# Kernel tuning notes

Hardware: AMD Instinct MI355X
Metric: run time of the kernel (lower is better)

The kernel has to match this reference:

```python
import jax, jax.numpy as jnp
import numpy as np

B, N, DIM = 2, 2048, 1024
H, DH = 16, 64
INNER = H * DH            # 1024
FF_INNER = 4 * DIM        # 4096
EPS = 1e-5


def _layer_norm(x, g, b):
    mu = jnp.mean(x, axis=-1, keepdims=True)
    var = jnp.mean(jnp.square(x - mu), axis=-1, keepdims=True)
    return (x - mu) * jax.lax.rsqrt(var + EPS) * g + b


def _self_attention(x, wq, wk, wv, wo, bo):
    # wq/wk/wv: [INNER, DIM] (torch Linear layout, y = x @ W^T)
    b, n, _ = x.shape
    q = jnp.einsum('bnd,id->bni', x, wq).reshape(b, n, H, DH).transpose(0, 2, 1, 3)
    k = jnp.einsum('bnd,id->bni', x, wk).reshape(b, n, H, DH).transpose(0, 2, 1, 3)
    v = jnp.einsum('bnd,id->bni', x, wv).reshape(b, n, H, DH).transpose(0, 2, 1, 3)
    scale = DH ** -0.5
    sim = jnp.einsum('bhid,bhjd->bhij', q, k) * scale   # [B,H,N,N]
    attn = jax.nn.softmax(sim, axis=-1)
    out = jnp.einsum('bhij,bhjd->bhid', attn, v)
    out = out.transpose(0, 2, 1, 3).reshape(b, n, INNER)
    return jnp.einsum('bni,di->bnd', out, wo) + bo


def _geglu_ff(x, w1, b1, w2, b2):
    # w1: [2*FF_INNER, DIM], w2: [DIM, FF_INNER]
    h = jnp.einsum('bnd,id->bni', x, w1) + b1
    a, gate = jnp.split(h, 2, axis=-1)
    h = a * jax.nn.gelu(gate, approximate=False)
    return jnp.einsum('bni,di->bnd', h, w2) + b2


def setup_inputs() -> dict:
    key = jax.random.key(0)
    ks = jax.random.split(key, 12)
    s = 0.02
    inp = {
        'x': jax.random.normal(ks[0], (B, N, DIM), jnp.float32),
        'ln1_g': jnp.ones((DIM,), jnp.float32),
        'ln1_b': jnp.zeros((DIM,), jnp.float32),
        'w_q1': jax.random.normal(ks[1], (INNER, DIM), jnp.float32) * s,
        'w_k1': jax.random.normal(ks[2], (INNER, DIM), jnp.float32) * s,
        'w_v1': jax.random.normal(ks[3], (INNER, DIM), jnp.float32) * s,
        'w_o1': jax.random.normal(ks[4], (DIM, INNER), jnp.float32) * s,
        'b_o1': jnp.zeros((DIM,), jnp.float32),
        'ln2_g': jnp.ones((DIM,), jnp.float32),
        'ln2_b': jnp.zeros((DIM,), jnp.float32),
        'w_q2': jax.random.normal(ks[5], (INNER, DIM), jnp.float32) * s,
        'w_k2': jax.random.normal(ks[6], (INNER, DIM), jnp.float32) * s,
        'w_v2': jax.random.normal(ks[7], (INNER, DIM), jnp.float32) * s,
        'w_o2': jax.random.normal(ks[8], (DIM, INNER), jnp.float32) * s,
        'b_o2': jnp.zeros((DIM,), jnp.float32),
        'ln3_g': jnp.ones((DIM,), jnp.float32),
        'ln3_b': jnp.zeros((DIM,), jnp.float32),
        'w_ff1': jax.random.normal(ks[9], (2 * FF_INNER, DIM), jnp.float32) * s,
        'b_ff1': jnp.zeros((2 * FF_INNER,), jnp.float32),
        'w_ff2': jax.random.normal(ks[10], (DIM, FF_INNER), jnp.float32) * s,
        'b_ff2': jnp.zeros((DIM,), jnp.float32),
    }
    return inp


def reference(x, ln1_g, ln1_b, w_q1, w_k1, w_v1, w_o1, b_o1,
              ln2_g, ln2_b, w_q2, w_k2, w_v2, w_o2, b_o2,
              ln3_g, ln3_b, w_ff1, b_ff1, w_ff2, b_ff2):
    # attn1 (self) + residual
    x = _self_attention(_layer_norm(x, ln1_g, ln1_b), w_q1, w_k1, w_v1, w_o1, b_o1) + x
    # attn2 (self, context=None) + residual
    x = _self_attention(_layer_norm(x, ln2_g, ln2_b), w_q2, w_k2, w_v2, w_o2, b_o2) + x
    # GEGLU feed-forward + residual
    x = _geglu_ff(_layer_norm(x, ln3_g, ln3_b), w_ff1, b_ff1, w_ff2, b_ff2) + x
    return x
```

## Files before the change

### kernel.cpp

```cpp
#include <hip/hip_runtime.h>
#include <hip/hip_bf16.h>

using bf16x8 = __attribute__((ext_vector_type(8))) short;
using f32x4  = __attribute__((ext_vector_type(4))) float;
using f32x16 = __attribute__((ext_vector_type(16))) float;
typedef unsigned int u32;
typedef unsigned short u16;
using u32x4 = __attribute__((ext_vector_type(4))) u32;

__device__ __forceinline__ u16 f2b(float f) {
  union { float f; u32 u; } v; v.f = f;
  return (u16)((v.u + 0x7FFFu + ((v.u >> 16) & 1u)) >> 16);
}

__device__ __forceinline__ u32 cvtpk(float lo, float hi) {
  u32 r;
  asm("v_cvt_pk_bf16_f32 %0, %1, %2" : "=v"(r) : "v"(lo), "v"(hi));
  return r;
}

__device__ __forceinline__ float exp2_raw(float x) {
  float r;
  asm("v_exp_f32 %0, %1" : "=v"(r) : "v"(x));
  return r;
}

__device__ __forceinline__ void gload16(const void* g, void* l) {
  __builtin_amdgcn_global_load_lds((const __attribute__((address_space(1))) u32*)g,
                                   (__attribute__((address_space(3))) u32*)l, 16, 0, 0);
}

__device__ __forceinline__ float gelu_fast(float x) {
  const float x2 = x * x;
  const float t = x * fmaf(0.044715f, x2, 1.f);
  const float u = exp2f(2.3022080f * t);
  return x * u * __builtin_amdgcn_rcpf(u + 1.f);
}

__global__ __launch_bounds__(256) void castall(
    const float* __restrict__ wq1, const float* __restrict__ wk1,
    const float* __restrict__ wv1, const float* __restrict__ wo1,
    const float* __restrict__ wq2, const float* __restrict__ wk2,
    const float* __restrict__ wv2, const float* __restrict__ wo2,
    const float* __restrict__ wff1, const float* __restrict__ wff2,
    u16* __restrict__ qkv1, u16* __restrict__ o1,
    u16* __restrict__ qkv2, u16* __restrict__ o2,
    u16* __restrict__ ff1p, u16* __restrict__ ff2) {
  const long e = ((long)blockIdx.x * 256 + threadIdx.x) * 4;
  constexpr long M1 = 1l << 20;
  const float* s; u16* d;
  if (e < 3 * M1) {
    s = (e < M1 ? wq1 + e : (e < 2 * M1 ? wk1 + (e - M1) : wv1 + (e - 2 * M1)));
    d = qkv1 + e;
  } else if (e < 4 * M1) {
    s = wo1 + (e - 3 * M1); d = o1 + (e - 3 * M1);
  } else if (e < 7 * M1) {
    long r = e - 4 * M1;
    s = (r < M1 ? wq2 + r : (r < 2 * M1 ? wk2 + (r - M1) : wv2 + (r - 2 * M1)));
    d = qkv2 + r;
  } else if (e < 8 * M1) {
    s = wo2 + (e - 7 * M1); d = o2 + (e - 7 * M1);
  } else if (e < 16 * M1) {
    long r = e - 8 * M1;
    long p = r >> 10, col = r & 1023;
    long g = p >> 5, rr = p & 31;
    long lr = (rr < 16) ? (g << 4) + rr : 4096 + (g << 4) + (rr - 16);
    s = wff1 + (lr << 10) + col; d = ff1p + r;
  } else {
    long r = e - 16 * M1;
    s = wff2 + r; d = ff2 + r;
  }
  float4 v = *(const float4*)s;
  ushort4 o;
  o.x = f2b(v.x); o.y = f2b(v.y); o.z = f2b(v.z); o.w = f2b(v.w);
  *(ushort4*)d = o;
}

__global__ __launch_bounds__(256) void ln_kernel(const float* __restrict__ x,
                                                 const float* __restrict__ g,
                                                 const float* __restrict__ b,
                                                 u16* __restrict__ y) {
  const int row = blockIdx.x;
  const int t = threadIdx.x;
  const float* xr = x + (size_t)row * 1024;
  float4 v = ((const float4*)xr)[t];
  float s  = v.x + v.y + v.z + v.w;
  float s2 = v.x * v.x + v.y * v.y + v.z * v.z + v.w * v.w;
  #pragma unroll
  for (int m = 1; m < 64; m <<= 1) {
    s  += __shfl_xor(s, m);
    s2 += __shfl_xor(s2, m);
  }
  __shared__ float red[8];
  if ((t & 63) == 0) { red[(t >> 6) * 2] = s; red[(t >> 6) * 2 + 1] = s2; }
  __syncthreads();
  s  = red[0] + red[2] + red[4] + red[6];
  s2 = red[1] + red[3] + red[5] + red[7];
  const float mu = s * (1.f / 1024.f);
  const float var = s2 * (1.f / 1024.f) - mu * mu;
  const float rs = rsqrtf(var + 1e-5f);
  float4 gv = ((const float4*)g)[t];
  float4 bv = ((const float4*)b)[t];
  ushort4 o;
  o.x = f2b((v.x - mu) * rs * gv.x + bv.x);
  o.y = f2b((v.y - mu) * rs * gv.y + bv.y);
  o.z = f2b((v.z - mu) * rs * gv.z + bv.z);
  o.w = f2b((v.w - mu) * rs * gv.w + bv.w);
  ((ushort4*)(y + (size_t)row * 1024))[t] = o;
}

__global__ __launch_bounds__(512, 4) void gemm_out(
    const u16* __restrict__ A, const u16* __restrict__ Bw,
    const float* __restrict__ bias, const float* __restrict__ resid,
    float* __restrict__ out, int N, int K) {
  extern __shared__ u16 lds[];
  const int tid = threadIdx.x;
  const int l = tid & 63, wid = tid >> 6;
  const int li = l & 15, lg = l >> 4;
  const int wr = wid >> 2, wc = wid & 3;
  const int nx = N >> 7;
  const int cpx = gridDim.x >> 3;
  const int v = (blockIdx.x & 7) * cpx + (blockIdx.x >> 3);
  const int by = v / nx, bx = v - by * nx;
  const int m0 = by << 7, n0 = bx << 7;

  const int sr = tid >> 3;
  const int sc = ((tid & 7) ^ (sr & 7)) << 3;
  const int dc = (tid & 7) << 3;
  const int sc0 = (lg * 8) ^ ((li & 7) << 3);
  const int sc1 = sc0 ^ 32;

  f32x4 acc[4][2] = {};

  auto stageA = [&](int kb, int t2) {
    #pragma unroll
    for (int s = 0; s < 2; ++s)
      gload16(A + (size_t)(m0 + s * 64 + sr) * K + t2 * 64 + sc,
              lds + kb * 8192 + (s * 64 + sr) * 64 + dc);
  };
  auto stageB = [&](int kb, int t2) {
    #pragma unroll
    for (int s = 0; s < 2; ++s)
      gload16(Bw + (size_t)(n0 + s * 64 + sr) * K + t2 * 64 + sc,
              lds + 16384 + kb * 8192 + (s * 64 + sr) * 64 + dc);
  };

  const int NT = K >> 6;
  stageA(0, 0); stageB(0, 0);
  __builtin_amdgcn_sched_barrier(0);
  stageA(1, 1); stageB(1, 1);
  __builtin_amdgcn_sched_barrier(0);
  asm volatile("s_waitcnt vmcnt(4)" ::: "memory");
  __builtin_amdgcn_s_barrier();
  __builtin_amdgcn_sched_barrier(0);

  for (int t = 0; t < NT; ++t) {
    const int kb = t & 1;
    const u16* Ab = lds + kb * 8192 + (wr * 64 + li) * 64;
    const u16* Bb = lds + 16384 + kb * 8192 + (wc * 32 + li) * 64;
    bf16x8 a[4], b[2];

    #pragma unroll
    for (int mi = 0; mi < 4; ++mi) a[mi] = *(const bf16x8*)(Ab + mi * 1024 + sc0);
    #pragma unroll
    for (int n = 0; n < 2; ++n)  b[n]  = *(const bf16x8*)(Bb + n * 1024 + sc0);
    __builtin_amdgcn_s_barrier();
    __builtin_amdgcn_s_setprio(1);
    #pragma unroll
    for (int mi = 0; mi < 4; ++mi)
      #pragma unroll
      for (int n = 0; n < 2; ++n)
        acc[mi][n] = __builtin_amdgcn_mfma_f32_16x16x32_bf16(a[mi], b[n], acc[mi][n], 0, 0, 0);
    __builtin_amdgcn_s_setprio(0);
    __builtin_amdgcn_s_barrier();

    #pragma unroll
    for (int mi = 0; mi < 4; ++mi) a[mi] = *(const bf16x8*)(Ab + mi * 1024 + sc1);
    #pragma unroll
    for (int n = 0; n < 2; ++n)  b[n]  = *(const bf16x8*)(Bb + n * 1024 + sc1);
    __builtin_amdgcn_s_barrier();
    __builtin_amdgcn_s_setprio(1);
    #pragma unroll
    for (int mi = 0; mi < 4; ++mi)
      #pragma unroll
      for (int n = 0; n < 2; ++n)
        acc[mi][n] = __builtin_amdgcn_mfma_f32_16x16x32_bf16(a[mi], b[n], acc[mi][n], 0, 0, 0);
    __builtin_amdgcn_s_setprio(0);
    if (t + 2 < NT) {
      stageA(kb, t + 2); stageB(kb, t + 2);
      asm volatile("s_waitcnt vmcnt(4)" ::: "memory");
    } else if (t + 2 == NT) {
      asm volatile("s_waitcnt vmcnt(0)" ::: "memory");
    }
    __builtin_amdgcn_s_barrier();
    __builtin_amdgcn_sched_barrier(0);
  }

  #pragma unroll
  for (int mi = 0; mi < 4; ++mi) {
    const int m = m0 + wr * 64 + mi * 16 + lg * 4;
    #pragma unroll
    for (int n = 0; n < 2; ++n) {
      const int j = n0 + wc * 32 + n * 16 + li;
      const float bj = bias[j];
      #pragma unroll
      for (int rb = 0; rb < 4; ++rb)
        out[(size_t)(m + rb) * N + j] =
            acc[mi][n][rb] + bj + resid[(size_t)(m + rb) * N + j];
    }
  }
}

#define KLOOP_PROLOGUE()                                                      \
  stageA(0, 0); stageB(0, 0); stageA(1, 0); stageB(1, 0);                     \
  __builtin_amdgcn_sched_barrier(0);                                          \
  stageA(0, 1); stageB(0, 1);                                                 \
  __builtin_amdgcn_sched_barrier(0);                                          \
  asm volatile("s_waitcnt vmcnt(4)" ::: "memory");                            \
  __builtin_amdgcn_s_barrier();                                               \
  __builtin_amdgcn_sched_barrier(0);

#define KLOOP_BODY(NT)                                                        \
  bf16x8 b0[4], b1[4];                                                        \
  for (int t = 0; t < NT; ++t) {                                              \
    const int kb = t & 1;                                                     \
    const u16* Abase0 = lds + (kb * 2 + 0) * 8192 + rowA0;                    \
    const u16* Abase1 = lds + (kb * 2 + 1) * 8192 + rowA0;                    \
    const u16* Bbase  = lds + (kb * 2 + bhn) * 8192 + rowB0;                  \
    bf16x8 a[4];                                                              \
                                                      \
    _Pragma("unroll")                                                         \
    for (int j = 0; j < 4; ++j) a[j]  = *(const bf16x8*)(Abase0 + j * 1024 + sc0); \
    _Pragma("unroll")                                                         \
    for (int n = 0; n < 4; ++n) b0[n] = *(const bf16x8*)(Bbase + n * 1024 + sc0); \
    if (t + 1 < NT) stageA(1, t + 1);                                         \
    __builtin_amdgcn_s_setprio(1);                                            \
    _Pragma("unroll")                                                         \
    for (int j = 0; j < 4; ++j)                                               \
      _Pragma("unroll")                                                       \
      for (int n = 0; n < 4; ++n)                                             \
        acc[j][n] = __builtin_amdgcn_mfma_f32_16x16x32_bf16(a[j], b0[n], acc[j][n], 0, 0, 0); \
    __builtin_amdgcn_s_setprio(0);                                            \
    __builtin_amdgcn_s_barrier();                                             \
                                                      \
    _Pragma("unroll")                                                         \
    for (int j = 0; j < 4; ++j) a[j]  = *(const bf16x8*)(Abase0 + j * 1024 + sc1); \
    _Pragma("unroll")                                                         \
    for (int n = 0; n < 4; ++n) b1[n] = *(const bf16x8*)(Bbase + n * 1024 + sc1); \
    if (t + 1 < NT) stageB(1, t + 1);                                         \
    __builtin_amdgcn_s_setprio(1);                                            \
    _Pragma("unroll")                                                         \
    for (int j = 0; j < 4; ++j)                                               \
      _Pragma("unroll")                                                       \
      for (int n = 0; n < 4; ++n)                                             \
        acc[j][n] = __builtin_amdgcn_mfma_f32_16x16x32_bf16(a[j], b1[n], acc[j][n], 0, 0, 0); \
    __builtin_amdgcn_s_setprio(0);                                            \
    __builtin_amdgcn_s_barrier();                                             \
                                                      \
    _Pragma("unroll")                                                         \
    for (int j = 0; j < 4; ++j) a[j] = *(const bf16x8*)(Abase1 + j * 1024 + sc0); \
    if (t + 2 < NT) stageA(0, t + 2);                                         \
    __builtin_amdgcn_s_setprio(1);                                            \
    _Pragma("unroll")                                                         \
    for (int j = 0; j < 4; ++j)                                               \
      _Pragma("unroll")                                                       \
      for (int n = 0; n < 4; ++n)                                             \
        acc[4 + j][n] = __builtin_amdgcn_mfma_f32_16x16x32_bf16(a[j], b0[n], acc[4 + j][n], 0, 0, 0); \
    __builtin_amdgcn_s_setprio(0);                                            \
    __builtin_amdgcn_s_barrier();                                             \
                                                      \
    _Pragma("unroll")                                                         \
    for (int j = 0; j < 4; ++j) a[j] = *(const bf16x8*)(Abase1 + j * 1024 + sc1); \
    if (t + 2 < NT) stageB(0, t + 2);                                         \
    __builtin_amdgcn_s_setprio(1);                                            \
    _Pragma("unroll")                                                         \
    for (int j = 0; j < 4; ++j)                                               \
      _Pragma("unroll")                                                       \
      for (int n = 0; n < 4; ++n)                                             \
        acc[4 + j][n] = __builtin_amdgcn_mfma_f32_16x16x32_bf16(a[j], b1[n], acc[4 + j][n], 0, 0, 0); \
    __builtin_amdgcn_s_setprio(0);                                            \
    if (t < NT - 2)       asm volatile("s_waitcnt vmcnt(4)" ::: "memory");    \
    else if (t == NT - 2) asm volatile("s_waitcnt vmcnt(0)" ::: "memory");    \
    __builtin_amdgcn_s_barrier();                                             \
  }

__global__ __launch_bounds__(512, 2) void gemm_ff1(
    const u16* __restrict__ A, const u16* __restrict__ Wp,
    const float* __restrict__ bias, u16* __restrict__ out) {
  extern __shared__ u16 lds[];
  const int tid = threadIdx.x;
  const int l = tid & 63, wid = tid >> 6;
  const int li = l & 15, lg = l >> 4;
  const int wr = wid >> 2, wc = wid & 3;
  const int xcd = blockIdx.x & 7, r = blockIdx.x >> 3;
  const int bx = (xcd & 3) * 8 + (r >> 3);
  const int by = (xcd >> 2) * 8 + (r & 7);

  const int lr8 = l >> 3;
  const int scb = ((l & 7) ^ lr8) << 3;
  const int sc0 = (lg * 8) ^ ((li & 7) << 3);
  const int sc1 = sc0 ^ 32;

  const int rowA0 = (wr * 64 + li) * 64;
  const int rowB0 = 32768 + ((wc & 1) * 64 + li) * 64;
  const int bhn = wc >> 1;

  f32x4 acc[8][4] = {};

  auto stageA = [&](int h, int t2) {
    const int kb2 = t2 & 1;
    #pragma unroll
    for (int s = 0; s < 2; ++s) {
      const u16* g = A + (size_t)(by * 256 + s * 128 + h * 64 + wid * 8 + lr8) * 1024
                       + t2 * 64 + scb;
      u16* d = lds + (kb2 * 2 + h) * 8192 + s * 4096 + wid * 512;
      gload16(g, d);
    }
  };
  auto stageB = [&](int h, int t2) {
    const int kb2 = t2 & 1;
    #pragma unroll
    for (int s = 0; s < 2; ++s) {
      const u16* g = Wp + (size_t)(bx * 256 + h * 128 + s * 64 + wid * 8 + lr8) * 1024
                        + t2 * 64 + scb;
      u16* d = lds + 32768 + (kb2 * 2 + h) * 8192 + s * 4096 + wid * 512;
      gload16(g, d);
    }
  };

  KLOOP_PROLOGUE()
  KLOOP_BODY(16)

  #pragma unroll
  for (int nj = 0; nj < 2; ++nj) {
    const int c = bx * 128 + wc * 32 + nj * 16 + li;
    const float ba = bias[c];
    const float bg = bias[4096 + c];
    #pragma unroll
    for (int mi = 0; mi < 8; ++mi) {
      #pragma unroll
      for (int rb = 0; rb < 4; ++rb) {
        const float av = acc[mi][2 * nj][rb] + ba;
        const float gv = acc[mi][2 * nj + 1][rb] + bg;
        out[(size_t)(by * 256 + wr * 128 + mi * 16 + lg * 4 + rb) * 4096 + c]
            = f2b(av * gelu_fast(gv));
      }
    }
  }
}

__global__ __launch_bounds__(512, 2) void gemm_qkv(
    const u16* __restrict__ A, const u16* __restrict__ Wp,
    u16* __restrict__ outp) {
  extern __shared__ u16 lds[];
  const int tid = threadIdx.x;
  const int l = tid & 63, wid = tid >> 6;
  const int li = l & 15, lg = l >> 4;
  const int wr = wid >> 2, wc = wid & 3;
  const int xcd = blockIdx.x & 7, r = blockIdx.x >> 3;
  const int by = (xcd >> 1) * 4 + r / 6;
  const int bx = (xcd & 1) * 6 + r % 6;

  const int lr8 = l >> 3;
  const int scb = ((l & 7) ^ lr8) << 3;
  const int sc0 = (lg * 8) ^ ((li & 7) << 3);
  const int sc1 = sc0 ^ 32;

  const int rowA0 = (wr * 64 + li) * 64;
  const int rowB0 = 32768 + ((wc & 1) * 64 + li) * 64;
  const int bhn = wc >> 1;

  f32x4 acc[8][4] = {};

  auto stageA = [&](int h, int t2) {
    const int kb2 = t2 & 1;
    #pragma unroll
    for (int s = 0; s < 2; ++s) {
      const u16* g = A + (size_t)(by * 256 + s * 128 + h * 64 + wid * 8 + lr8) * 1024
                       + t2 * 64 + scb;
      u16* d = lds + (kb2 * 2 + h) * 8192 + s * 4096 + wid * 512;
      gload16(g, d);
    }
  };
  auto stageB = [&](int h, int t2) {
    const int kb2 = t2 & 1;
    #pragma unroll
    for (int s = 0; s < 2; ++s) {
      const u16* g = Wp + (size_t)(bx * 256 + h * 128 + s * 64 + wid * 8 + lr8) * 1024
                        + t2 * 64 + scb;
      u16* d = lds + 32768 + (kb2 * 2 + h) * 8192 + s * 4096 + wid * 512;
      gload16(g, d);
    }
  };

  KLOOP_PROLOGUE()
  KLOOP_BODY(16)

  #pragma unroll
  for (int mi = 0; mi < 8; ++mi) {
    const int mbase = by * 256 + wr * 128 + mi * 16 + lg * 4;
    #pragma unroll
    for (int ni = 0; ni < 4; ++ni) {
      const int j = bx * 256 + wc * 64 + ni * 16 + li;
      f32x4 a = acc[mi][ni];
      const int sec = j >> 10, jj = j & 1023;
      const int h = jj >> 6, dd = jj & 63;
      u16* base = outp + (size_t)sec * 4194304;
      if (sec == 0) {
        #pragma unroll
        for (int rb = 0; rb < 4; ++rb) {
          const int m = mbase + rb;
          const int bb = m >> 11, n = m & 2047;
          base[(((size_t)bb * 16 + h) * 2048 + n) * 64 + dd] =
              f2b(a[rb] * 0.18033688011112042f);
        }
      } else if (sec == 1) {
        #pragma unroll
        for (int rb = 0; rb < 4; ++rb) {
          const int m = mbase + rb;
          const int bb = m >> 11, n = m & 2047;
          base[(((size_t)bb * 16 + h) * 2048 + n) * 64 + (dd ^ ((n & 7) << 3))] =
              f2b(a[rb]);
        }
      } else {
        const int bb = mbase >> 11, n = mbase & 2047;
        const int ng = n & ~63, nl = n & 63;
        const int nl2 = (nl & 51) | ((nl & 4) << 1) | ((nl & 8) >> 1);
        const int col = ng | (nl2 ^ ((dd & 7) << 3));
        ushort4 pk;
        pk.x = f2b(a[0]); pk.y = f2b(a[1]); pk.z = f2b(a[2]); pk.w = f2b(a[3]);
        *(ushort4*)&base[(((size_t)bb * 16 + h) * 64 + dd) * 2048 + col] = pk;
      }
    }
  }
}

__global__ __launch_bounds__(256, 2) void attn_fwd(
    const u16* __restrict__ Q, const u16* __restrict__ K,
    const u16* __restrict__ Vt, u16* __restrict__ Out) {
  __shared__ u16 smem[4][8192];
  const int tid = threadIdx.x;
  const int l = tid & 63, w = tid >> 6;
  const int lo = l & 31, hi = l >> 5, l7 = l & 7;
  const int bh = blockIdx.x & 31, qt = blockIdx.x >> 5;
  const int b_ = bh >> 4, h = bh & 15;

  const u16* Qg = Q + ((size_t)bh * 2048 + qt * 128 + w * 32 + lo) * 64;
  const u16* Kg = K + (size_t)bh * 2048 * 64;
  const u16* Vg = Vt + (size_t)bh * 64 * 2048;

  bf16x8 qf[4];
  #pragma unroll
  for (int d = 0; d < 4; ++d) qf[d] = *(const bf16x8*)&Qg[d * 16 + hi * 8];

  const bf16x8 onesf = {(short)0x3F80, (short)0x3F80, (short)0x3F80, (short)0x3F80,
                        (short)0x3F80, (short)0x3F80, (short)0x3F80, (short)0x3F80};

  f32x16 o0 = {}, o1 = {}, lacc = {};

  auto stage = [&](int buf, int jt) {
    #pragma unroll
    for (int i = 0; i < 2; ++i)
      gload16(Kg + (size_t)jt * 4096 + i * 2048 + tid * 8,
              &smem[buf][i * 2048 + w * 512]);
    #pragma unroll
    for (int i = 0; i < 2; ++i)
      gload16(Vg + (size_t)(w * 8 + (l >> 3) + i * 32) * 2048 + jt * 64 + l7 * 8,
              &smem[buf][4096 + i * 2048 + w * 512]);
  };

  __builtin_amdgcn_sched_barrier(0);
  stage(0, 0);
  __builtin_amdgcn_sched_barrier(0);
  stage(1, 1);
  __builtin_amdgcn_sched_barrier(0);
  stage(2, 2);
  __builtin_amdgcn_sched_barrier(0);

  for (int jt = 0; jt < 32; ++jt) {
    if (jt < 30)       asm volatile("s_waitcnt vmcnt(8)" ::: "memory");
    else if (jt == 30) asm volatile("s_waitcnt vmcnt(4)" ::: "memory");
    else               asm volatile("s_waitcnt vmcnt(0)" ::: "memory");
    __builtin_amdgcn_s_barrier();
    __builtin_amdgcn_sched_barrier(0);
    if (jt + 3 < 32) stage((jt + 3) & 3, jt + 3);

    const u16* Kl = &smem[jt & 3][0];
    const u16* Vl = &smem[jt & 3][4096];

    bf16x8 kf[4][2], vf0[4], vf1[4];
    #pragma unroll
    for (int dc = 0; dc < 4; ++dc) {
      const int col = (dc * 16 + hi * 8) ^ (l7 << 3);
      kf[dc][0] = *(const bf16x8*)&Kl[lo * 64 + col];
      kf[dc][1] = *(const bf16x8*)&Kl[(32 + lo) * 64 + col];
      vf0[dc]   = *(const bf16x8*)&Vl[lo * 64 + col];
      vf1[dc]   = *(const bf16x8*)&Vl[(32 + lo) * 64 + col];
    }

    f32x16 st[2] = {};
    __builtin_amdgcn_s_setprio(1);
    #pragma unroll
    for (int dc = 0; dc < 4; ++dc) {
      st[0] = __builtin_amdgcn_mfma_f32_32x32x16_bf16(kf[dc][0], qf[dc], st[0], 0, 0, 0);
      st[1] = __builtin_amdgcn_mfma_f32_32x32x16_bf16(kf[dc][1], qf[dc], st[1], 0, 0, 0);
    }
    __builtin_amdgcn_s_setprio(0);

    float p[32];
    #pragma unroll
    for (int r = 0; r < 16; ++r) p[r]      = exp2_raw(st[0][r] - 8.f);
    #pragma unroll
    for (int r = 0; r < 16; ++r) p[16 + r] = exp2_raw(st[1][r] - 8.f);

    bf16x8 pf[4];
    #pragma unroll
    for (int kp = 0; kp < 4; ++kp) {
      u32x4 wv;
      #pragma unroll
      for (int t2 = 0; t2 < 4; ++t2)
        wv[t2] = cvtpk(p[(kp >> 1) * 16 + (kp & 1) * 8 + t2 * 2],
                       p[(kp >> 1) * 16 + (kp & 1) * 8 + t2 * 2 + 1]);
      union { u32x4 a; bf16x8 b; } cc; cc.a = wv;
      pf[kp] = cc.b;
    }

    __builtin_amdgcn_s_setprio(1);
    #pragma unroll
    for (int kp = 0; kp < 4; ++kp) {
      o0   = __builtin_amdgcn_mfma_f32_32x32x16_bf16(vf0[kp], pf[kp], o0, 0, 0, 0);
      o1   = __builtin_amdgcn_mfma_f32_32x32x16_bf16(vf1[kp], pf[kp], o1, 0, 0, 0);
      lacc = __builtin_amdgcn_mfma_f32_32x32x16_bf16(onesf,   pf[kp], lacc, 0, 0, 0);
    }
    __builtin_amdgcn_s_setprio(0);
  }

  const float inv = 1.f / lacc[0];
  u16* Ob = Out + ((size_t)b_ * 2048 + qt * 128 + w * 32 + lo) * 1024 + h * 64;
  #pragma unroll
  for (int dd = 0; dd < 2; ++dd) {
    #pragma unroll
    for (int R = 0; R < 4; ++R) {
      ushort4 pk;
      const f32x16 oo = dd ? o1 : o0;
      pk.x = f2b(oo[4 * R + 0] * inv); pk.y = f2b(oo[4 * R + 1] * inv);
      pk.z = f2b(oo[4 * R + 2] * inv); pk.w = f2b(oo[4 * R + 3] * inv);
      *(ushort4*)&Ob[dd * 32 + 8 * R + 4 * hi] = pk;
    }
  }
}

extern "C" void kernel_launch(void* const* d_in, const int* in_sizes, int n_in,
                              void* d_out, int out_size, void* d_ws, size_t ws_size,
                              hipStream_t stream) {
  const float* x    = (const float*)d_in[0];
  const float* ln1g = (const float*)d_in[1];
  const float* ln1b = (const float*)d_in[2];
  const float* wq1  = (const float*)d_in[3];
  const float* wk1  = (const float*)d_in[4];
  const float* wv1  = (const float*)d_in[5];
  const float* wo1  = (const float*)d_in[6];
  const float* bo1  = (const float*)d_in[7];
  const float* ln2g = (const float*)d_in[8];
  const float* ln2b = (const float*)d_in[9];
  const float* wq2  = (const float*)d_in[10];
  const float* wk2  = (const float*)d_in[11];
  const float* wv2  = (const float*)d_in[12];
  const float* wo2  = (const float*)d_in[13];
  const float* bo2  = (const float*)d_in[14];
  const float* ln3g = (const float*)d_in[15];
  const float* ln3b = (const float*)d_in[16];
  const float* wff1 = (const float*)d_in[17];
  const float* bff1 = (const float*)d_in[18];
  const float* wff2 = (const float*)d_in[19];
  const float* bff2 = (const float*)d_in[20];

  char* ws = (char*)d_ws;
  const size_t MB = 1024 * 1024;
  u16* wqkv1b = (u16*)(ws + 0 * MB);
  u16* wo1b   = (u16*)(ws + 6 * MB);
  u16* wqkv2b = (u16*)(ws + 8 * MB);
  u16* wo2b   = (u16*)(ws + 14 * MB);
  u16* wff1p  = (u16*)(ws + 16 * MB);
  u16* wff2b  = (u16*)(ws + 32 * MB);
  u16* xn     = (u16*)(ws + 40 * MB);
  u16* Qb     = (u16*)(ws + 48 * MB);
  float* x1   = (float*)(ws + 72 * MB);
  float* x2   = (float*)(ws + 88 * MB);
  u16* hact   = (u16*)(ws + 48 * MB);
  u16* Kb  = Qb + 4194304;
  u16* Vtb = Qb + 8388608;

  hipFuncSetAttribute((const void*)gemm_ff1,
                      hipFuncAttributeMaxDynamicSharedMemorySize, 131072);
  hipFuncSetAttribute((const void*)gemm_qkv,
                      hipFuncAttributeMaxDynamicSharedMemorySize, 131072);
  hipFuncSetAttribute((const void*)gemm_out,
                      hipFuncAttributeMaxDynamicSharedMemorySize, 65536);

  castall<<<20480, 256, 0, stream>>>(wq1, wk1, wv1, wo1, wq2, wk2, wv2, wo2,
                                     wff1, wff2,
                                     wqkv1b, wo1b, wqkv2b, wo2b, wff1p, wff2b);

  ln_kernel<<<4096, 256, 0, stream>>>(x, ln1g, ln1b, xn);
  gemm_qkv<<<192, 512, 131072, stream>>>(xn, wqkv1b, Qb);
  attn_fwd<<<512, 256, 0, stream>>>(Qb, Kb, Vtb, xn);
  gemm_out<<<256, 512, 65536, stream>>>(xn, wo1b, bo1, x, x1, 1024, 1024);

  ln_kernel<<<4096, 256, 0, stream>>>(x1, ln2g, ln2b, xn);
  gemm_qkv<<<192, 512, 131072, stream>>>(xn, wqkv2b, Qb);
  attn_fwd<<<512, 256, 0, stream>>>(Qb, Kb, Vtb, xn);
  gemm_out<<<256, 512, 65536, stream>>>(xn, wo2b, bo2, x1, x2, 1024, 1024);

  ln_kernel<<<4096, 256, 0, stream>>>(x2, ln3g, ln3b, xn);
  gemm_ff1<<<512, 512, 131072, stream>>>(xn, wff1p, bff1, hact);
  gemm_out<<<256, 512, 65536, stream>>>(hact, wff2b, bff2, x2, (float*)d_out, 1024, 4096);
}
```

Measured before the change: 359.9 us.

## Rewrite attention kernel with 16x16 MFMA tiles, smaller blocks and double buffering

The attention kernel moves from 32x32x16 to 16x16x32 bf16 MFMAs. Each block now covers 64 query rows instead of 128, so the grid doubles to 1024 blocks. The K/V LDS ring shrinks from four stages to two, and launch bounds rise to four blocks per CU. The V-transpose layout in the QKV GEMM changes to match the new fragment ordering. The aim is to cut register and LDS pressure for higher occupancy, at the cost of a shallower prefetch pipeline (a full vmcnt(0) wait each tile) and K/V reloaded by twice as many blocks.

```diff
diff --git a/kernel.cpp b/kernel.cpp
--- a/kernel.cpp
+++ b/kernel.cpp
@@ -3,7 +3,6 @@
 
 using bf16x8 = __attribute__((ext_vector_type(8))) short;
 using f32x4  = __attribute__((ext_vector_type(4))) float;
-using f32x16 = __attribute__((ext_vector_type(16))) float;
 typedef unsigned int u32;
 typedef unsigned short u16;
 using u32x4 = __attribute__((ext_vector_type(4))) u32;
@@ -425,8 +424,8 @@
       } else {
         const int bb = mbase >> 11, n = mbase & 2047;
         const int ng = n & ~63, nl = n & 63;
-        const int nl2 = (nl & 51) | ((nl & 4) << 1) | ((nl & 8) >> 1);
-        const int col = ng | (nl2 ^ ((dd & 7) << 3));
+        const int slot = (nl & 3) | ((nl & 12) << 1) | ((nl & 16) >> 2) | (nl & 32);
+        const int col = ng | (slot ^ ((dd & 7) << 3));
         ushort4 pk;
         pk.x = f2b(a[0]); pk.y = f2b(a[1]); pk.z = f2b(a[2]); pk.w = f2b(a[3]);
         *(ushort4*)&base[(((size_t)bb * 16 + h) * 64 + dd) * 2048 + col] = pk;
@@ -435,28 +434,28 @@
   }
 }
 
-__global__ __launch_bounds__(256, 2) void attn_fwd(
+__global__ __launch_bounds__(256, 4) void attn_fwd(
     const u16* __restrict__ Q, const u16* __restrict__ K,
     const u16* __restrict__ Vt, u16* __restrict__ Out) {
-  __shared__ u16 smem[4][8192];
+  __shared__ u16 smem[2][8192];
   const int tid = threadIdx.x;
   const int l = tid & 63, w = tid >> 6;
-  const int lo = l & 31, hi = l >> 5, l7 = l & 7;
+  const int li = l & 15, hi4 = l >> 4, l7 = l & 7;
   const int bh = blockIdx.x & 31, qt = blockIdx.x >> 5;
   const int b_ = bh >> 4, h = bh & 15;
 
-  const u16* Qg = Q + ((size_t)bh * 2048 + qt * 128 + w * 32 + lo) * 64;
+  const u16* Qg = Q + ((size_t)bh * 2048 + qt * 64 + w * 16 + li) * 64;
   const u16* Kg = K + (size_t)bh * 2048 * 64;
   const u16* Vg = Vt + (size_t)bh * 64 * 2048;
 
-  bf16x8 qf[4];
-  #pragma unroll
-  for (int d = 0; d < 4; ++d) qf[d] = *(const bf16x8*)&Qg[d * 16 + hi * 8];
+  const bf16x8 qf0 = *(const bf16x8*)&Qg[hi4 * 8];
+  const bf16x8 qf1 = *(const bf16x8*)&Qg[32 + hi4 * 8];
 
   const bf16x8 onesf = {(short)0x3F80, (short)0x3F80, (short)0x3F80, (short)0x3F80,
                         (short)0x3F80, (short)0x3F80, (short)0x3F80, (short)0x3F80};
 
-  f32x16 o0 = {}, o1 = {}, lacc = {};
+  f32x4 o[4] = {};
+  f32x4 lacc = {};
 
   auto stage = [&](int buf, int jt) {
     #pragma unroll
@@ -469,84 +468,70 @@
               &smem[buf][4096 + i * 2048 + w * 512]);
   };
 
-  __builtin_amdgcn_sched_barrier(0);
   stage(0, 0);
-  __builtin_amdgcn_sched_barrier(0);
-  stage(1, 1);
-  __builtin_amdgcn_sched_barrier(0);
-  stage(2, 2);
-  __builtin_amdgcn_sched_barrier(0);
 
   for (int jt = 0; jt < 32; ++jt) {
-    if (jt < 30)       asm volatile("s_waitcnt vmcnt(8)" ::: "memory");
-    else if (jt == 30) asm volatile("s_waitcnt vmcnt(4)" ::: "memory");
-    else               asm volatile("s_waitcnt vmcnt(0)" ::: "memory");
+    const int cur = jt & 1;
+    asm volatile("s_waitcnt vmcnt(0)" ::: "memory");
     __builtin_amdgcn_s_barrier();
     __builtin_amdgcn_sched_barrier(0);
-    if (jt + 3 < 32) stage((jt + 3) & 3, jt + 3);
-
-    const u16* Kl = &smem[jt & 3][0];
-    const u16* Vl = &smem[jt & 3][4096];
-
-    bf16x8 kf[4][2], vf0[4], vf1[4];
+    if (jt + 1 < 32) stage(cur ^ 1, jt + 1);
+
+    const u16* Kl = &smem[cur][0];
+    const u16* Vl = &smem[cur][4096];
+    const int c0 = (hi4 * 8) ^ (l7 << 3);
+    const int c1 = (32 + hi4 * 8) ^ (l7 << 3);
+
+    f32x4 st[4] = {};
+    __builtin_amdgcn_s_setprio(1);
+    #pragma unroll
+    for (int g = 0; g < 4; ++g) {
+      const bf16x8 kf0 = *(const bf16x8*)&Kl[(g * 16 + li) * 64 + c0];
+      const bf16x8 kf1 = *(const bf16x8*)&Kl[(g * 16 + li) * 64 + c1];
+      st[g] = __builtin_amdgcn_mfma_f32_16x16x32_bf16(kf0, qf0, st[g], 0, 0, 0);
+      st[g] = __builtin_amdgcn_mfma_f32_16x16x32_bf16(kf1, qf1, st[g], 0, 0, 0);
+    }
+    __builtin_amdgcn_s_setprio(0);
+
+    float p[16];
+    #pragma unroll
+    for (int g = 0; g < 4; ++g)
+      #pragma unroll
+      for (int r = 0; r < 4; ++r)
+        p[g * 4 + r] = exp2_raw(st[g][r] - 8.f);
+
+    u32x4 w0, w1;
+    #pragma unroll
+    for (int t2 = 0; t2 < 4; ++t2) {
+      w0[t2] = cvtpk(p[t2 * 2], p[t2 * 2 + 1]);
+      w1[t2] = cvtpk(p[8 + t2 * 2], p[8 + t2 * 2 + 1]);
+    }
+    union { u32x4 a; bf16x8 b; } cc0, cc1;
+    cc0.a = w0; cc1.a = w1;
+    const bf16x8 pf0 = cc0.b, pf1 = cc1.b;
+
+    __builtin_amdgcn_s_setprio(1);
     #pragma unroll
     for (int dc = 0; dc < 4; ++dc) {
-      const int col = (dc * 16 + hi * 8) ^ (l7 << 3);
-      kf[dc][0] = *(const bf16x8*)&Kl[lo * 64 + col];
-      kf[dc][1] = *(const bf16x8*)&Kl[(32 + lo) * 64 + col];
-      vf0[dc]   = *(const bf16x8*)&Vl[lo * 64 + col];
-      vf1[dc]   = *(const bf16x8*)&Vl[(32 + lo) * 64 + col];
-    }
-
-    f32x16 st[2] = {};
-    __builtin_amdgcn_s_setprio(1);
-    #pragma unroll
-    for (int dc = 0; dc < 4; ++dc) {
-      st[0] = __builtin_amdgcn_mfma_f32_32x32x16_bf16(kf[dc][0], qf[dc], st[0], 0, 0, 0);
-      st[1] = __builtin_amdgcn_mfma_f32_32x32x16_bf16(kf[dc][1], qf[dc], st[1], 0, 0, 0);
-    }
+      const bf16x8 vf0 = *(const bf16x8*)&Vl[(dc * 16 + li) * 64 + c0];
+      const bf16x8 vf1 = *(const bf16x8*)&Vl[(dc * 16 + li) * 64 + c1];
+      o[dc] = __builtin_amdgcn_mfma_f32_16x16x32_bf16(vf0, pf0, o[dc], 0, 0, 0);
+      o[dc] = __builtin_amdgcn_mfma_f32_16x16x32_bf16(vf1, pf1, o[dc], 0, 0, 0);
+    }
+    lacc = __builtin_amdgcn_mfma_f32_16x16x32_bf16(onesf, pf0, lacc, 0, 0, 0);
+    lacc = __builtin_amdgcn_mfma_f32_16x16x32_bf16(onesf, pf1, lacc, 0, 0, 0);
     __builtin_amdgcn_s_setprio(0);
-
-    float p[32];
-    #pragma unroll
-    for (int r = 0; r < 16; ++r) p[r]      = exp2_raw(st[0][r] - 8.f);
-    #pragma unroll
-    for (int r = 0; r < 16; ++r) p[16 + r] = exp2_raw(st[1][r] - 8.f);
-
-    bf16x8 pf[4];
-    #pragma unroll
-    for (int kp = 0; kp < 4; ++kp) {
-      u32x4 wv;
-      #pragma unroll
-      for (int t2 = 0; t2 < 4; ++t2)
-        wv[t2] = cvtpk(p[(kp >> 1) * 16 + (kp & 1) * 8 + t2 * 2],
-                       p[(kp >> 1) * 16 + (kp & 1) * 8 + t2 * 2 + 1]);
-      union { u32x4 a; bf16x8 b; } cc; cc.a = wv;
-      pf[kp] = cc.b;
-    }
-
-    __builtin_amdgcn_s_setprio(1);
-    #pragma unroll
-    for (int kp = 0; kp < 4; ++kp) {
-      o0   = __builtin_amdgcn_mfma_f32_32x32x16_bf16(vf0[kp], pf[kp], o0, 0, 0, 0);
-      o1   = __builtin_amdgcn_mfma_f32_32x32x16_bf16(vf1[kp], pf[kp], o1, 0, 0, 0);
-      lacc = __builtin_amdgcn_mfma_f32_32x32x16_bf16(onesf,   pf[kp], lacc, 0, 0, 0);
-    }
-    __builtin_amdgcn_s_setprio(0);
   }
 
   const float inv = 1.f / lacc[0];
-  u16* Ob = Out + ((size_t)b_ * 2048 + qt * 128 + w * 32 + lo) * 1024 + h * 64;
+  const int q = qt * 64 + w * 16 + li;
+  u16* Ob = Out + ((size_t)b_ * 2048 + q) * 1024 + h * 64;
   #pragma unroll
-  for (int dd = 0; dd < 2; ++dd) {
-    #pragma unroll
-    for (int R = 0; R < 4; ++R) {
-      ushort4 pk;
-      const f32x16 oo = dd ? o1 : o0;
-      pk.x = f2b(oo[4 * R + 0] * inv); pk.y = f2b(oo[4 * R + 1] * inv);
-      pk.z = f2b(oo[4 * R + 2] * inv); pk.w = f2b(oo[4 * R + 3] * inv);
-      *(ushort4*)&Ob[dd * 32 + 8 * R + 4 * hi] = pk;
-    }
+  for (int dc = 0; dc < 4; ++dc) {
+    ushort4 pk;
+    pk.x = f2b(o[dc][0] * inv); pk.y = f2b(o[dc][1] * inv);
+    pk.z = f2b(o[dc][2] * inv); pk.w = f2b(o[dc][3] * inv);
+    *(ushort4*)&Ob[dc * 16 + hi4 * 4] = pk;
   }
 }
 
@@ -604,12 +589,12 @@
 
   ln_kernel<<<4096, 256, 0, stream>>>(x, ln1g, ln1b, xn);
   gemm_qkv<<<192, 512, 131072, stream>>>(xn, wqkv1b, Qb);
-  attn_fwd<<<512, 256, 0, stream>>>(Qb, Kb, Vtb, xn);
+  attn_fwd<<<1024, 256, 0, stream>>>(Qb, Kb, Vtb, xn);
   gemm_out<<<256, 512, 65536, stream>>>(xn, wo1b, bo1, x, x1, 1024, 1024);
 
   ln_kernel<<<4096, 256, 0, stream>>>(x1, ln2g, ln2b, xn);
   gemm_qkv<<<192, 512, 131072, stream>>>(xn, wqkv2b, Qb);
-  attn_fwd<<<512, 256, 0, stream>>>(Qb, Kb, Vtb, xn);
+  attn_fwd<<<1024, 256, 0, stream>>>(Qb, Kb, Vtb, xn);
   gemm_out<<<256, 512, 65536, stream>>>(xn, wo2b, bo2, x1, x2, 1024, 1024);
 
   ln_kernel<<<4096, 256, 0, stream>>>(x2, ln3g, ln3b, xn);
```

New measurement: 347.3 us. -3.5%, faster.
